# Kernel tuning notes

Measured on AMD Instinct MI355X. Metric: run time of the kernel, lower is better.

The kernel has to match this reference:

```python
import jax, jax.numpy as jnp
import numpy as np

W_DIM = 512
C_IN = 512
C_OUT = 512
K = 3
EPS = 1e-6
STYLE_SCALE = 1.0 / np.sqrt(W_DIM)              # EqualizedWeight scale for (out,in)
CONV_SCALE = 1.0 / np.sqrt(C_IN * K * K)        # EqualizedWeight scale for (out,in,k,k)


def setup_inputs() -> dict:
    key = jax.random.key(0)
    ks = jax.random.split(key, 6)
    B, H, W = 16, 64, 64
    return {
        "x": jax.random.normal(ks[0], (B, C_IN, H, W), dtype=jnp.float32),
        "w": jax.random.normal(ks[1], (B, W_DIM), dtype=jnp.float32),
        "style_weight": jax.random.normal(ks[2], (C_IN, W_DIM), dtype=jnp.float32),
        "style_bias": jnp.zeros((C_IN,), dtype=jnp.float32),
        "conv_weight": jax.random.normal(ks[3], (C_OUT, C_IN, K, K), dtype=jnp.float32),
        "noise_weight": jax.random.normal(ks[4], (1, C_OUT, 1, 1), dtype=jnp.float32),
        "bias": jnp.zeros((C_OUT,), dtype=jnp.float32),
        "noise": jax.random.normal(ks[5], (B, 1, H, W), dtype=jnp.float32),
    }


def reference(x, w, style_weight, style_bias, conv_weight, noise_weight, bias, noise):
    B, _, H, Wd = x.shape
    # to_style: equalized linear  [B, C_IN]
    s = w @ (style_weight * STYLE_SCALE).T + style_bias
    # modulate: [B, C_OUT, C_IN, K, K]
    wts = (conv_weight * CONV_SCALE)[None] * s[:, None, :, None, None]
    # demodulate
    sigma = jax.lax.rsqrt(jnp.sum(wts * wts, axis=(2, 3, 4)) + EPS)  # [B, C_OUT]
    wts = wts * sigma[:, :, None, None, None]
    # grouped conv with groups = batch
    x_r = x.reshape(1, B * C_IN, H, Wd)
    w_r = wts.reshape(B * C_OUT, C_IN, K, K)
    y = jax.lax.conv_general_dilated(
        x_r, w_r, window_strides=(1, 1), padding=[(1, 1), (1, 1)],
        dimension_numbers=("NCHW", "OIHW", "NCHW"), feature_group_count=B,
    ).reshape(B, C_OUT, H, Wd)
    # noise injection + bias + leaky relu(0.2)
    y = y + noise_weight * noise + bias[None, :, None, None]
    return jax.nn.leaky_relu(y, negative_slope=0.2)
```

## Files before the change

kernel.cpp:

```cpp
#include <hip/hip_runtime.h>


typedef __attribute__((ext_vector_type(8))) short short8;
typedef __attribute__((ext_vector_type(4))) float f32x4;

#define STYLE_SCALE 0.044194173824159216f
#define CONV_SCALE  0.014731391274719742f
#define CS2         (1.0f/4608.0f)

static __device__ __forceinline__ unsigned short f2bf(float x) {
    union { float f; unsigned int u; } a; a.f = x;
    unsigned int r = a.u + 0x7fffu + ((a.u >> 16) & 1u);
    return (unsigned short)(r >> 16);
}

static __device__ __forceinline__ void gl_lds16(const void* g, void* l) {
    __builtin_amdgcn_global_load_lds(
        (const __attribute__((address_space(1))) unsigned int*)g,
        (__attribute__((address_space(3))) unsigned int*)l, 16, 0, 0);
}

__global__ void k_style(const float* __restrict__ w, const float* __restrict__ sw,
                        const float* __restrict__ sb, float* __restrict__ s) {
    int b = blockIdx.y, j0 = blockIdx.x * 64, t = threadIdx.x;
    __shared__ float wl[512];
    __shared__ float part[256];
    wl[t] = w[b*512 + t]; wl[t+256] = w[b*512 + t + 256];
    __syncthreads();
    int jl = t & 63, seg = t >> 6;
    const float4* row = (const float4*)(sw + (size_t)(j0 + jl)*512) + seg*32;
    const float*  wv  = wl + seg*128;
    float acc = 0.f;
#pragma unroll 4
    for (int k = 0; k < 32; ++k) {
        float4 v = row[k];
        acc += v.x*wv[4*k] + v.y*wv[4*k+1] + v.z*wv[4*k+2] + v.w*wv[4*k+3];
    }
    part[t] = acc;
    __syncthreads();
    if (t < 64)
        s[b*512 + j0 + t] = (part[t] + part[t+64] + part[t+128] + part[t+192])
                            * STYLE_SCALE + sb[j0 + t];
}

__global__ void k_wprep(const float* __restrict__ cw, float* __restrict__ csq,
                        unsigned short* __restrict__ cwt) {
    int o = blockIdx.x, t = threadIdx.x;
    __shared__ float row[4608];
    const float4* src = (const float4*)(cw + (size_t)o*4608);
    for (int i = t; i < 1152; i += 256) ((float4*)row)[i] = src[i];
    __syncthreads();
#pragma unroll
    for (int it = 0; it < 2; ++it) {
        int i = t + it*256;
        float a = 0.f;
#pragma unroll
        for (int k = 0; k < 9; ++k) { float v = row[i*9 + k]; a += v*v; }
        csq[(size_t)o*512 + i] = a * CS2;
    }
    for (int p = t; p < 576; p += 256) {
        int ic = p / 36, rem = p % 36;
        int tap = rem >> 2, g = rem & 3;
        int i0 = ic*32 + g*8;
        union { unsigned short us[8]; uint4 q; } u;
#pragma unroll
        for (int j = 0; j < 8; ++j)
            u.us[j] = f2bf(row[(i0 + j)*9 + tap] * CONV_SCALE);
        *(uint4*)(cwt + ((size_t)p*512 + o)*8) = u.q;
    }
}

__global__ void k_sigma(const float* __restrict__ s, const float* __restrict__ csq,
                        float* __restrict__ sig) {
    int b = blockIdx.y, o0 = blockIdx.x * 64, t = threadIdx.x;
    __shared__ float s2l[512];
    __shared__ float part[256];
    float v0 = s[b*512 + t], v1 = s[b*512 + t + 256];
    s2l[t] = v0*v0; s2l[t+256] = v1*v1;
    __syncthreads();
    int ol = t & 63, seg = t >> 6;
    const float4* row = (const float4*)(csq + (size_t)(o0 + ol)*512) + seg*32;
    const float*  sv  = s2l + seg*128;
    float acc = 0.f;
#pragma unroll 4
    for (int k = 0; k < 32; ++k) {
        float4 c = row[k];
        acc += c.x*sv[4*k] + c.y*sv[4*k+1] + c.z*sv[4*k+2] + c.w*sv[4*k+3];
    }
    part[t] = acc;
    __syncthreads();
    if (t < 64)
        sig[b*512 + o0 + t] = 1.0f / sqrtf(part[t] + part[t+64] + part[t+128]
                                           + part[t+192] + 1e-6f);
}

__global__ void k_xt(const float* __restrict__ x, const float* __restrict__ s,
                     unsigned short* __restrict__ xt) {
    int h = blockIdx.x, b = blockIdx.y, t = threadIdx.x;
    __shared__ float tile[64][65];
    __shared__ float sl[64];
    for (int c0 = 0; c0 < 512; c0 += 64) {
        if (t < 64) sl[t] = s[b*512 + c0 + t];
#pragma unroll
        for (int it = 0; it < 4; ++it) {
            int idx = t + it*256;
            int c = idx >> 4, w4 = (idx & 15) * 4;
            float4 v = *(const float4*)(x + ((size_t)(b*512 + c0 + c)*4096) + h*64 + w4);
            tile[c][w4]   = v.x; tile[c][w4+1] = v.y;
            tile[c][w4+2] = v.z; tile[c][w4+3] = v.w;
        }
        __syncthreads();
#pragma unroll
        for (int it = 0; it < 2; ++it) {
            int idx = t + it*256;
            int wq = idx >> 3, c = (idx & 7) * 8;
            union { unsigned short us[8]; uint4 q; } u;
#pragma unroll
            for (int j = 0; j < 8; ++j)
                u.us[j] = f2bf(tile[c + j][wq] * sl[c + j]);
            *(uint4*)(xt + ((size_t)(b*4096 + h*64 + wq)*512 + c0 + c)) = u.q;
        }
        __syncthreads();
    }
}

__global__ __launch_bounds__(256, 2)
void k_conv(const unsigned short* __restrict__ xt, const unsigned short* __restrict__ cwt,
            const float* __restrict__ sig, const float* __restrict__ nw,
            const float* __restrict__ bias, const float* __restrict__ noise,
            float* __restrict__ out) {
    __shared__ short xs_s[10*66*32];
    __shared__ short wsm_s[9*4*64*8];

    const int tid  = threadIdx.x;
    const int lane = tid & 63;
    const int wave = tid >> 6;
    const int quad = lane >> 4;
    const int l15  = lane & 15;

    const int b     = blockIdx.y;
    const int oblk  = blockIdx.x & 7;
    const int pxblk = blockIdx.x >> 3;
    const int o0 = oblk * 64, h0 = pxblk * 8;

    for (int i = tid; i < 10*66*32/2; i += 256) ((unsigned int*)xs_s)[i] = 0u;
    __syncthreads();

    f32x4 acc[2][4][4];
#pragma unroll
    for (int rr = 0; rr < 2; ++rr)
#pragma unroll
        for (int mt = 0; mt < 4; ++mt)
#pragma unroll
            for (int nt = 0; nt < 4; ++nt) acc[rr][mt][nt] = (f32x4){0.f,0.f,0.f,0.f};

    const short8* wp = (const short8*)wsm_s;
    const short8* xp = (const short8*)xs_s;

    for (int ic = 0; ic < 16; ++ic) {
        for (int q = wave; q < 76; q += 4) {
            if (q < 36) {
                const unsigned short* src = cwt + ((size_t)(ic*36 + q)*512 + o0 + lane)*8;
                gl_lds16(src, wsm_s + q*512);
            } else {
                int xq = q - 36;
                int r = xq >> 2, p0 = (xq & 3) << 4;
                int gr = h0 - 1 + r;
                if (gr >= 0 && gr < 64) {
                    int p  = p0 + (lane >> 2);
                    int cg = (lane & 3) ^ ((lane >> 2) & 3);
                    const unsigned short* src =
                        xt + ((size_t)(b*4096 + gr*64 + p)*512 + ic*32 + cg*8);
                    gl_lds16(src, xs_s + (r*66 + 1 + p0)*32);
                }
            }
        }
        __syncthreads();

#pragma unroll
        for (int dx = 0; dx < 3; ++dx) {
            const int col0 = l15 + dx;
            const int slot = quad ^ ((l15 + dx - 1) & 3);
            const short8* xbase = xp + slot;
            short8 bufA[4], bufB[4];

#define LOADB(buf, d) do {                                                  \
            int rbase = ((2*wave + (d))*66 + col0) * 4;                     \
            buf[0] = xbase[rbase];        buf[1] = xbase[rbase + 64];       \
            buf[2] = xbase[rbase + 128];  buf[3] = xbase[rbase + 192];      \
        } while (0)

#define TAPSTEP(dy, C0, C1) do {                                            \
            const int tap = (dy)*3 + dx;                                    \
            short8 af[4];                                                   \
            _Pragma("unroll")                                               \
            for (int mt = 0; mt < 4; ++mt)                                  \
                af[mt] = wp[(tap*4 + quad)*64 + mt*16 + l15];               \
            _Pragma("unroll")                                               \
            for (int mt = 0; mt < 4; ++mt) {                                \
                _Pragma("unroll")                                           \
                for (int nt = 0; nt < 4; ++nt) {                            \
                    acc[0][mt][nt] = __builtin_amdgcn_mfma_f32_16x16x32_bf16( \
                        af[mt], C0[nt], acc[0][mt][nt], 0, 0, 0);           \
                    acc[1][mt][nt] = __builtin_amdgcn_mfma_f32_16x16x32_bf16( \
                        af[mt], C1[nt], acc[1][mt][nt], 0, 0, 0);           \
                }                                                           \
            }                                                               \
        } while (0)

            LOADB(bufA, 0);
            LOADB(bufB, 1);
            TAPSTEP(0, bufA, bufB);
            LOADB(bufA, 2);
            TAPSTEP(1, bufB, bufA);
            LOADB(bufB, 3);
            TAPSTEP(2, bufA, bufB);
#undef LOADB
#undef TAPSTEP
        }
        __syncthreads();
    }

    float nz[2][4];
#pragma unroll
    for (int rr = 0; rr < 2; ++rr) {
        int h = h0 + 2*wave + rr;
#pragma unroll
        for (int nt = 0; nt < 4; ++nt) nz[rr][nt] = noise[b*4096 + h*64 + nt*16 + l15];
    }
#pragma unroll
    for (int mt = 0; mt < 4; ++mt) {
#pragma unroll
        for (int r = 0; r < 4; ++r) {
            int o = o0 + mt*16 + quad*4 + r;
            float sg  = sig[b*512 + o];
            float nwv = nw[o], bv = bias[o];
#pragma unroll
            for (int rr = 0; rr < 2; ++rr) {
                int h = h0 + 2*wave + rr;
#pragma unroll
                for (int nt = 0; nt < 4; ++nt) {
                    float v = acc[rr][mt][nt][r] * sg + nwv * nz[rr][nt] + bv;
                    v = (v >= 0.f) ? v : 0.2f * v;
                    out[((size_t)(b*512 + o)*4096) + h*64 + nt*16 + l15] = v;
                }
            }
        }
    }
}

extern "C" void kernel_launch(void* const* d_in, const int* in_sizes, int n_in,
                              void* d_out, int out_size, void* d_ws, size_t ws_size,
                              hipStream_t stream) {
    const float* x     = (const float*)d_in[0];
    const float* w     = (const float*)d_in[1];
    const float* sw    = (const float*)d_in[2];
    const float* sb    = (const float*)d_in[3];
    const float* cw    = (const float*)d_in[4];
    const float* nw    = (const float*)d_in[5];
    const float* bias  = (const float*)d_in[6];
    const float* noise = (const float*)d_in[7];
    float* out = (float*)d_out;

    char* ws = (char*)d_ws;
    unsigned short* xt  = (unsigned short*)(ws + 0);
    unsigned short* cwt = (unsigned short*)(ws + 67108864);
    float* s   = (float*)(ws + 71827456);
    float* sig = (float*)(ws + 71860224);
    float* csq = (float*)(ws + 71892992);

    k_wprep<<<512, 256, 0, stream>>>(cw, csq, cwt);
    k_style<<<dim3(8, 16), 256, 0, stream>>>(w, sw, sb, s);
    k_sigma<<<dim3(8, 16), 256, 0, stream>>>(s, csq, sig);
    k_xt   <<<dim3(64, 16), 256, 0, stream>>>(x, s, xt);
    k_conv <<<dim3(64, 16), 256, 0, stream>>>(xt, cwt, sig, nw, bias, noise, out);
}
```

Measured before the change: 498.2 us.

## Double-buffer activation tiles, read weights from global, swizzle block order

The conv kernel now double-buffers the activation tile in LDS, prefetching the next channel chunk while computing the current one. The weight tile is no longer staged in LDS and is read straight from global memory into registers. The padded halo columns are removed, and edge columns are zeroed in registers. The grid is flattened and remapped so consecutive blocks spread across batch and pixel tiles, which may help cache locality. The cost is extra global weight traffic and more register pressure, with some risk of exposed load latency.

```diff
diff --git a/kernel.cpp b/kernel.cpp
--- a/kernel.cpp
+++ b/kernel.cpp
@@ -129,8 +129,7 @@
             const float* __restrict__ sig, const float* __restrict__ nw,
             const float* __restrict__ bias, const float* __restrict__ noise,
             float* __restrict__ out) {
-    __shared__ short xs_s[10*66*32];
-    __shared__ short wsm_s[9*4*64*8];
+    __shared__ __align__(16) short xs_s[2][20480];
 
     const int tid  = threadIdx.x;
     const int lane = tid & 63;
@@ -138,13 +137,35 @@
     const int quad = lane >> 4;
     const int l15  = lane & 15;
 
-    const int b     = blockIdx.y;
-    const int oblk  = blockIdx.x & 7;
-    const int pxblk = blockIdx.x >> 3;
+    const int flat = blockIdx.x;
+    const int nf   = (flat & 7) * 128 + (flat >> 3);
+    const int oblk = nf & 7, pxblk = (nf >> 3) & 7, b = nf >> 6;
     const int o0 = oblk * 64, h0 = pxblk * 8;
 
-    for (int i = tid; i < 10*66*32/2; i += 256) ((unsigned int*)xs_s)[i] = 0u;
-    __syncthreads();
+    if (h0 == 0)
+        for (int i = tid; i < 1024; i += 256) {
+            ((unsigned int*)xs_s[0])[i] = 0u;
+            ((unsigned int*)xs_s[1])[i] = 0u;
+        }
+    if (h0 == 56)
+        for (int i = tid; i < 1024; i += 256) {
+            ((unsigned int*)xs_s[0])[9*1024 + i] = 0u;
+            ((unsigned int*)xs_s[1])[9*1024 + i] = 0u;
+        }
+
+    const int pp = lane >> 2;
+    const int cg = (lane & 3) ^ (pp & 3) ^ ((pp >> 2) & 3);
+
+#define STAGE(bufidx, icn) do {                                              \
+        short* dst_ = xs_s[bufidx];                                          \
+        for (int q_ = wave; q_ < 40; q_ += 4) {                              \
+            int r_ = q_ >> 2, p0_ = (q_ & 3) << 4;                           \
+            int gr_ = h0 - 1 + r_;                                           \
+            if (gr_ >= 0 && gr_ < 64)                                        \
+                gl_lds16(xt + ((size_t)(b*4096 + gr_*64 + p0_ + pp)*512      \
+                               + (icn)*32 + cg*8),                           \
+                         dst_ + (r_*64 + p0_)*32);                           \
+        } } while (0)
 
     f32x4 acc[2][4][4];
 #pragma unroll
@@ -154,72 +175,74 @@
 #pragma unroll
             for (int nt = 0; nt < 4; ++nt) acc[rr][mt][nt] = (f32x4){0.f,0.f,0.f,0.f};
 
-    const short8* wp = (const short8*)wsm_s;
-    const short8* xp = (const short8*)xs_s;
+    const unsigned short* cwth = cwt + (size_t)quad*4096 + (size_t)(o0 + l15)*8;
+
+    STAGE(0, 0);
+    __syncthreads();
 
     for (int ic = 0; ic < 16; ++ic) {
-        for (int q = wave; q < 76; q += 4) {
-            if (q < 36) {
-                const unsigned short* src = cwt + ((size_t)(ic*36 + q)*512 + o0 + lane)*8;
-                gl_lds16(src, wsm_s + q*512);
-            } else {
-                int xq = q - 36;
-                int r = xq >> 2, p0 = (xq & 3) << 4;
-                int gr = h0 - 1 + r;
-                if (gr >= 0 && gr < 64) {
-                    int p  = p0 + (lane >> 2);
-                    int cg = (lane & 3) ^ ((lane >> 2) & 3);
-                    const unsigned short* src =
-                        xt + ((size_t)(b*4096 + gr*64 + p)*512 + ic*32 + cg*8);
-                    gl_lds16(src, xs_s + (r*66 + 1 + p0)*32);
-                }
-            }
-        }
+        if (ic < 15) STAGE((ic + 1) & 1, ic + 1);
+
+        const short8* xp = (const short8*)xs_s[ic & 1];
+        const unsigned short* cwA = cwth + (size_t)ic * 147456;
+        const short8 z8 = {};
+
+#define LOADA(dst, tap) do { _Pragma("unroll")                               \
+        for (int mt_ = 0; mt_ < 4; ++mt_)                                    \
+            dst[mt_] = *(const short8*)(cwA + (size_t)(tap)*16384 + mt_*128);\
+        } while (0)
+
+#define TAPSTEP(AF, C0, C1) do { _Pragma("unroll")                           \
+        for (int mt_ = 0; mt_ < 4; ++mt_) { _Pragma("unroll")                \
+            for (int nt_ = 0; nt_ < 4; ++nt_) {                              \
+                acc[0][mt_][nt_] = __builtin_amdgcn_mfma_f32_16x16x32_bf16(  \
+                    AF[mt_], C0[nt_], acc[0][mt_][nt_], 0, 0, 0);            \
+                acc[1][mt_][nt_] = __builtin_amdgcn_mfma_f32_16x16x32_bf16(  \
+                    AF[mt_], C1[nt_], acc[1][mt_][nt_], 0, 0, 0);            \
+            } } } while (0)
+
+#pragma unroll
+        for (int dx = 0; dx < 3; ++dx) {
+            const int cs   = l15 + dx + 15;
+            const int slot = quad ^ (cs & 3) ^ ((cs >> 2) & 3);
+            const int colS = cs*4 + slot;
+
+#define LOADB(bf, d) do {                                                    \
+            const int base_ = (2*wave + (d))*256 + colS;                     \
+            if (dx == 0) {                                                   \
+                int a0_ = (l15 == 0) ? base_ : base_ - 64;                   \
+                bf[0] = xp[a0_];        bf[1] = xp[base_];                   \
+                bf[2] = xp[base_ + 64]; bf[3] = xp[base_ + 128];             \
+                if (l15 == 0) bf[0] = z8;                                    \
+            } else if (dx == 1) {                                            \
+                bf[0] = xp[base_ - 64]; bf[1] = xp[base_];                   \
+                bf[2] = xp[base_ + 64]; bf[3] = xp[base_ + 128];             \
+            } else {                                                         \
+                int a3_ = (l15 == 15) ? base_ : base_ + 128;                 \
+                bf[0] = xp[base_ - 64]; bf[1] = xp[base_];                   \
+                bf[2] = xp[base_ + 64]; bf[3] = xp[a3_];                     \
+                if (l15 == 15) bf[3] = z8;                                   \
+            }                                                                \
+        } while (0)
+
+            short8 afA[4], afB[4], bA[4], bB[4];
+            LOADA(afA, dx);
+            LOADA(afB, dx + 3);
+            LOADB(bA, 0);
+            LOADB(bB, 1);
+            TAPSTEP(afA, bA, bB);
+            LOADA(afA, dx + 6);
+            LOADB(bA, 2);
+            TAPSTEP(afB, bB, bA);
+            LOADB(bB, 3);
+            TAPSTEP(afA, bA, bB);
+#undef LOADB
+        }
+#undef LOADA
+#undef TAPSTEP
         __syncthreads();
-
-#pragma unroll
-        for (int dx = 0; dx < 3; ++dx) {
-            const int col0 = l15 + dx;
-            const int slot = quad ^ ((l15 + dx - 1) & 3);
-            const short8* xbase = xp + slot;
-            short8 bufA[4], bufB[4];
-
-#define LOADB(buf, d) do {                                                  \
-            int rbase = ((2*wave + (d))*66 + col0) * 4;                     \
-            buf[0] = xbase[rbase];        buf[1] = xbase[rbase + 64];       \
-            buf[2] = xbase[rbase + 128];  buf[3] = xbase[rbase + 192];      \
-        } while (0)
-
-#define TAPSTEP(dy, C0, C1) do {                                            \
-            const int tap = (dy)*3 + dx;                                    \
-            short8 af[4];                                                   \
-            _Pragma("unroll")                                               \
-            for (int mt = 0; mt < 4; ++mt)                                  \
-                af[mt] = wp[(tap*4 + quad)*64 + mt*16 + l15];               \
-            _Pragma("unroll")                                               \
-            for (int mt = 0; mt < 4; ++mt) {                                \
-                _Pragma("unroll")                                           \
-                for (int nt = 0; nt < 4; ++nt) {                            \
-                    acc[0][mt][nt] = __builtin_amdgcn_mfma_f32_16x16x32_bf16( \
-                        af[mt], C0[nt], acc[0][mt][nt], 0, 0, 0);           \
-                    acc[1][mt][nt] = __builtin_amdgcn_mfma_f32_16x16x32_bf16( \
-                        af[mt], C1[nt], acc[1][mt][nt], 0, 0, 0);           \
-                }                                                           \
-            }                                                               \
-        } while (0)
-
-            LOADB(bufA, 0);
-            LOADB(bufB, 1);
-            TAPSTEP(0, bufA, bufB);
-            LOADB(bufA, 2);
-            TAPSTEP(1, bufB, bufA);
-            LOADB(bufB, 3);
-            TAPSTEP(2, bufA, bufB);
-#undef LOADB
-#undef TAPSTEP
-        }
-        __syncthreads();
-    }
+    }
+#undef STAGE
 
     float nz[2][4];
 #pragma unroll
@@ -273,5 +296,5 @@
     k_style<<<dim3(8, 16), 256, 0, stream>>>(w, sw, sb, s);
     k_sigma<<<dim3(8, 16), 256, 0, stream>>>(s, csq, sig);
     k_xt   <<<dim3(64, 16), 256, 0, stream>>>(x, s, xt);
-    k_conv <<<dim3(64, 16), 256, 0, stream>>>(xt, cwt, sig, nw, bias, noise, out);
-}
+    k_conv <<<dim3(1024), 256, 0, stream>>>(xt, cwt, sig, nw, bias, noise, out);
+}
```

Result: no change. 492.2 us (-1.2%).
